# Performance work log

Hardware: AMD Instinct MI355X
Metric: run time of the kernel (lower is better)

Reference implementation:

```python
import jax, jax.numpy as jnp
import numpy as np

KH, KW = 3, 3
H_OUT, W_OUT = 62, 62

def setup_inputs() -> dict:
    key = jax.random.key(0)
    k1, k2 = jax.random.split(key)
    x = jax.random.normal(k1, (16, 32, 64, 64), dtype=jnp.float32)
    weight = jax.random.normal(k2, (H_OUT, W_OUT, 64, 32, KH, KW), dtype=jnp.float32) * 0.01
    return {"x": x, "weight": weight}

def reference(x, weight):
    # Unfold: patches[b,c,kh,kw,i,j] = x[b,c,i+kh,j+kw]; small fixed 3x3 loop is fine.
    patches = jnp.stack([
        jnp.stack([x[:, :, kh:kh + H_OUT, kw:kw + W_OUT] for kw in range(KW)], axis=2)
        for kh in range(KH)
    ], axis=2)  # [B, C_in, kH, kW, H_out, W_out]
    # Per-position (no weight sharing) contraction over c_in, kh, kw.
    out = jnp.einsum('bcklij,ijockl->boij', patches, weight)
    return jax.nn.sigmoid(out)
```

## Files before the change

kernel.cpp:

```cpp
#include <hip/hip_runtime.h>

#define HO 62
#define WO 62
#define CIN 32
#define COUT 64
#define BATCH 16
#define KROW 288
#define JT 4
#define COLS 6

typedef float f4a4 __attribute__((ext_vector_type(4), aligned(4)));

__global__ __launch_bounds__(256, 4)
void lc2d_kernel(const float* __restrict__ x,
                 const float* __restrict__ wgt,
                 float* __restrict__ out) {
    __shared__ __align__(16) float win[CIN][3][COLS][BATCH];

    const int blk = blockIdx.x;
    const int i  = blk % HO;
    const int j0 = (blk / HO) * JT;

    const int t = threadIdx.x;

    for (int r = t; r < BATCH * CIN * 3; r += 256) {
        const int b   = r & 15;
        const int ckh = r >> 4;
        const int c   = ckh / 3;
        const int kh  = ckh % 3;
        const float* src = x + (((b * CIN + c) * 64) + (i + kh)) * 64;
        #pragma unroll
        for (int cc = 0; cc < COLS; cc++) {
            int col = j0 + cc;
            if (col > 63) col = 63;
            win[c][kh][cc][b] = src[col];
        }
    }
    __syncthreads();

    const int wsel = t >> 6;
    const int o    = t & 63;

    const float* wj[JT];
    #pragma unroll
    for (int jj = 0; jj < JT; jj++) {
        int pj = i * WO + (j0 + jj);
        if (pj > HO * WO - 1) pj = HO * WO - 1;
        wj[jj] = wgt + (size_t)pj * (COUT * KROW) + o * KROW;
    }

    float acc[JT][4];
    #pragma unroll
    for (int jj = 0; jj < JT; jj++)
        #pragma unroll
        for (int bb = 0; bb < 4; bb++) acc[jj][bb] = 0.0f;

    const float* xbase = &win[0][0][0][wsel * 4];

    for (int c = 0; c < CIN; c++) {
        float wq[JT][9];
        #pragma unroll
        for (int jj = 0; jj < JT; jj++) {
            const float* p = wj[jj] + c * 9;
            const f4a4 wA = *(const f4a4*)p;
            const f4a4 wB = *(const f4a4*)(p + 4);
            wq[jj][0] = wA.x; wq[jj][1] = wA.y; wq[jj][2] = wA.z; wq[jj][3] = wA.w;
            wq[jj][4] = wB.x; wq[jj][5] = wB.y; wq[jj][6] = wB.z; wq[jj][7] = wB.w;
            wq[jj][8] = p[8];
        }
        #pragma unroll
        for (int kh = 0; kh < 3; kh++) {
            float4 xv[COLS];
            const float* xb = xbase + (c * 3 + kh) * (COLS * BATCH);
            #pragma unroll
            for (int cc = 0; cc < COLS; cc++)
                xv[cc] = *(const float4*)(xb + cc * BATCH);
            #pragma unroll
            for (int jj = 0; jj < JT; jj++) {
                #pragma unroll
                for (int kw = 0; kw < 3; kw++) {
                    const float w = wq[jj][kh * 3 + kw];
                    const float4 xx = xv[jj + kw];
                    acc[jj][0] += w * xx.x;
                    acc[jj][1] += w * xx.y;
                    acc[jj][2] += w * xx.z;
                    acc[jj][3] += w * xx.w;
                }
            }
        }
    }

    #pragma unroll
    for (int bb = 0; bb < 4; bb++) {
        const int b = wsel * 4 + bb;
        float* op = out + (((size_t)(b * COUT + o) * HO + i) * WO + j0);
        float2 s0;
        s0.x = 1.0f / (1.0f + __expf(-acc[0][bb]));
        s0.y = 1.0f / (1.0f + __expf(-acc[1][bb]));
        *(float2*)op = s0;
        if (j0 + 3 < WO) {
            float2 s1;
            s1.x = 1.0f / (1.0f + __expf(-acc[2][bb]));
            s1.y = 1.0f / (1.0f + __expf(-acc[3][bb]));
            *((float2*)op + 1) = s1;
        }
    }
}

extern "C" void kernel_launch(void* const* d_in, const int* in_sizes, int n_in,
                              void* d_out, int out_size, void* d_ws, size_t ws_size,
                              hipStream_t stream) {
    const float* x   = (const float*)d_in[0];
    const float* wgt = (const float*)d_in[1];
    float* out       = (float*)d_out;
    const int grid = HO * ((WO + JT - 1) / JT);
    lc2d_kernel<<<dim3(grid), dim3(256), 0, stream>>>(x, wgt, out);
}
```

Measured before the change: 572.0 us.

## Stage weights through double-buffered LDS with coalesced loads and two-column tiles

Weights are no longer read straight from global memory by each thread with strided per-output-channel loads. Each block now cooperatively loads 36-float chunks of the weight slab into double-buffered, padded shared memory with coalesced float4 loads, prefetching the next chunk while computing on the current one. The column tile shrinks from four to two so the grid divides evenly and no clamping is needed. This targets the weight-bandwidth-bound stream, at the cost of per-chunk syncs, more LDS use, lower occupancy and more blocks.

```diff
diff --git a/kernel.cpp b/kernel.cpp
--- a/kernel.cpp
+++ b/kernel.cpp
@@ -6,104 +6,133 @@
 #define COUT 64
 #define BATCH 16
 #define KROW 288
-#define JT 4
-#define COLS 6
+#define JT 2
+#define COLS 4
+#define NCHUNK 8
+#define CF 36
+#define WROW 37
+#define POSW (COUT * WROW)
 
-typedef float f4a4 __attribute__((ext_vector_type(4), aligned(4)));
+__device__ __forceinline__ float sigmoidf(float v) {
+    return 1.0f / (1.0f + __expf(-v));
+}
 
-__global__ __launch_bounds__(256, 4)
+__global__ __launch_bounds__(256, 2)
 void lc2d_kernel(const float* __restrict__ x,
                  const float* __restrict__ wgt,
                  float* __restrict__ out) {
     __shared__ __align__(16) float win[CIN][3][COLS][BATCH];
+    __shared__ __align__(16) float wlds[2][JT][POSW];
 
     const int blk = blockIdx.x;
     const int i  = blk % HO;
     const int j0 = (blk / HO) * JT;
-
-    const int t = threadIdx.x;
+    const int t  = threadIdx.x;
 
     for (int r = t; r < BATCH * CIN * 3; r += 256) {
         const int b   = r & 15;
         const int ckh = r >> 4;
         const int c   = ckh / 3;
-        const int kh  = ckh % 3;
-        const float* src = x + (((b * CIN + c) * 64) + (i + kh)) * 64;
+        const int kh  = ckh - c * 3;
+        const float* src = x + (((b * CIN + c) * 64) + (i + kh)) * 64 + j0;
         #pragma unroll
-        for (int cc = 0; cc < COLS; cc++) {
-            int col = j0 + cc;
-            if (col > 63) col = 63;
-            win[c][kh][cc][b] = src[col];
+        for (int cc = 0; cc < COLS; cc++)
+            win[c][kh][cc][b] = src[cc];
+    }
+
+    const int nq = (t < 128) ? 5 : 4;
+    int goff[5], loff[5];
+    #pragma unroll
+    for (int q = 0; q < 5; q++) {
+        int f = t + 256 * q;
+        if (f >= 1152) f = 1151;
+        const int pos = f / 576;
+        const int rem = f - pos * 576;
+        const int o   = rem / 9;
+        const int kk4 = rem - o * 9;
+        goff[q] = pos * (COUT * KROW) + o * KROW + kk4 * 4;
+        loff[q] = pos * POSW + o * WROW + kk4 * 4;
+    }
+    const float* wslab = wgt + (size_t)(i * WO + j0) * (COUT * KROW);
+
+    float4 st[5];
+
+    #pragma unroll
+    for (int q = 0; q < 5; q++)
+        if (q < nq) st[q] = *(const float4*)(wslab + goff[q]);
+    #pragma unroll
+    for (int q = 0; q < 5; q++)
+        if (q < nq) {
+            float* d = &wlds[0][0][0] + loff[q];
+            d[0] = st[q].x; d[1] = st[q].y; d[2] = st[q].z; d[3] = st[q].w;
         }
-    }
     __syncthreads();
 
     const int wsel = t >> 6;
     const int o    = t & 63;
+    const int bq4  = wsel * 4;
 
-    const float* wj[JT];
+    float acc0[4] = {0.f, 0.f, 0.f, 0.f};
+    float acc1[4] = {0.f, 0.f, 0.f, 0.f};
+
     #pragma unroll
-    for (int jj = 0; jj < JT; jj++) {
-        int pj = i * WO + (j0 + jj);
-        if (pj > HO * WO - 1) pj = HO * WO - 1;
-        wj[jj] = wgt + (size_t)pj * (COUT * KROW) + o * KROW;
-    }
+    for (int ch = 0; ch < NCHUNK; ch++) {
+        const int cur = ch & 1;
 
-    float acc[JT][4];
-    #pragma unroll
-    for (int jj = 0; jj < JT; jj++)
+        if (ch + 1 < NCHUNK) {
+            #pragma unroll
+            for (int q = 0; q < 5; q++)
+                if (q < nq) st[q] = *(const float4*)(wslab + goff[q] + (ch + 1) * CF);
+        }
+
+        const float* w0p = &wlds[cur][0][0] + o * WROW;
+        const float* w1p = &wlds[cur][1][0] + o * WROW;
+        float w0[CF], w1[CF];
         #pragma unroll
-        for (int bb = 0; bb < 4; bb++) acc[jj][bb] = 0.0f;
+        for (int m = 0; m < CF; m++) { w0[m] = w0p[m]; w1[m] = w1p[m]; }
 
-    const float* xbase = &win[0][0][0][wsel * 4];
-
-    for (int c = 0; c < CIN; c++) {
-        float wq[JT][9];
+        const int c0 = ch * 4;
         #pragma unroll
-        for (int jj = 0; jj < JT; jj++) {
-            const float* p = wj[jj] + c * 9;
-            const f4a4 wA = *(const f4a4*)p;
-            const f4a4 wB = *(const f4a4*)(p + 4);
-            wq[jj][0] = wA.x; wq[jj][1] = wA.y; wq[jj][2] = wA.z; wq[jj][3] = wA.w;
-            wq[jj][4] = wB.x; wq[jj][5] = wB.y; wq[jj][6] = wB.z; wq[jj][7] = wB.w;
-            wq[jj][8] = p[8];
-        }
-        #pragma unroll
-        for (int kh = 0; kh < 3; kh++) {
-            float4 xv[COLS];
-            const float* xb = xbase + (c * 3 + kh) * (COLS * BATCH);
+        for (int cl = 0; cl < 4; cl++) {
             #pragma unroll
-            for (int cc = 0; cc < COLS; cc++)
-                xv[cc] = *(const float4*)(xb + cc * BATCH);
-            #pragma unroll
-            for (int jj = 0; jj < JT; jj++) {
+            for (int kh = 0; kh < 3; kh++) {
+                const float* xb = &win[c0 + cl][kh][0][bq4];
+                float4 xv[COLS];
+                #pragma unroll
+                for (int cc = 0; cc < COLS; cc++)
+                    xv[cc] = *(const float4*)(xb + cc * BATCH);
                 #pragma unroll
                 for (int kw = 0; kw < 3; kw++) {
-                    const float w = wq[jj][kh * 3 + kw];
-                    const float4 xx = xv[jj + kw];
-                    acc[jj][0] += w * xx.x;
-                    acc[jj][1] += w * xx.y;
-                    acc[jj][2] += w * xx.z;
-                    acc[jj][3] += w * xx.w;
+                    const float wa = w0[cl * 9 + kh * 3 + kw];
+                    const float wb = w1[cl * 9 + kh * 3 + kw];
+                    acc0[0] += wa * xv[kw].x;     acc0[1] += wa * xv[kw].y;
+                    acc0[2] += wa * xv[kw].z;     acc0[3] += wa * xv[kw].w;
+                    acc1[0] += wb * xv[kw + 1].x; acc1[1] += wb * xv[kw + 1].y;
+                    acc1[2] += wb * xv[kw + 1].z; acc1[3] += wb * xv[kw + 1].w;
                 }
             }
+        }
+
+        if (ch + 1 < NCHUNK) {
+            float* base = &wlds[cur ^ 1][0][0];
+            #pragma unroll
+            for (int q = 0; q < 5; q++)
+                if (q < nq) {
+                    float* d = base + loff[q];
+                    d[0] = st[q].x; d[1] = st[q].y; d[2] = st[q].z; d[3] = st[q].w;
+                }
+            __syncthreads();
         }
     }
 
     #pragma unroll
     for (int bb = 0; bb < 4; bb++) {
-        const int b = wsel * 4 + bb;
+        const int b = bq4 + bb;
         float* op = out + (((size_t)(b * COUT + o) * HO + i) * WO + j0);
-        float2 s0;
-        s0.x = 1.0f / (1.0f + __expf(-acc[0][bb]));
-        s0.y = 1.0f / (1.0f + __expf(-acc[1][bb]));
-        *(float2*)op = s0;
-        if (j0 + 3 < WO) {
-            float2 s1;
-            s1.x = 1.0f / (1.0f + __expf(-acc[2][bb]));
-            s1.y = 1.0f / (1.0f + __expf(-acc[3][bb]));
-            *((float2*)op + 1) = s1;
-        }
+        float2 s;
+        s.x = sigmoidf(acc0[bb]);
+        s.y = sigmoidf(acc1[bb]);
+        *(float2*)op = s;
     }
 }
 
@@ -113,6 +142,6 @@
     const float* x   = (const float*)d_in[0];
     const float* wgt = (const float*)d_in[1];
     float* out       = (float*)d_out;
-    const int grid = HO * ((WO + JT - 1) / JT);
+    const int grid = HO * (WO / JT);
     lc2d_kernel<<<dim3(grid), dim3(256), 0, stream>>>(x, wgt, out);
 }
```

After: 2.226 ms. 289% more time.

## Stage weights through LDS in double-buffered chunks with coalesced global loads

Applied to the files above, without the earlier changes.

Weights were previously read straight from global memory, with each thread pulling its own 9-float row slices. Now each block loads the 288-float weight rows for its 4 output positions into shared memory in 8 chunks of 4 input channels, using contiguous 16-byte loads. The next chunk's weights and input window are prefetched into registers while the current chunk is computed. Threads are remapped so each handles one position and four output channels, and launch bounds drop to 3 waves per SIMD. The cost is more shared memory, two barriers per chunk, scalar uncoalesced output stores, and extra register pressure.

```diff
diff --git a/kernel.cpp b/kernel.cpp
--- a/kernel.cpp
+++ b/kernel.cpp
@@ -4,105 +4,155 @@
 #define WO 62
 #define CIN 32
 #define COUT 64
-#define BATCH 16
-#define KROW 288
+#define NB 16
+#define KR 288
 #define JT 4
-#define COLS 6
+#define NCH 8
+#define WROW 36
 
-typedef float f4a4 __attribute__((ext_vector_type(4), aligned(4)));
+typedef float f2 __attribute__((ext_vector_type(2)));
+typedef float f4 __attribute__((ext_vector_type(4)));
 
-__global__ __launch_bounds__(256, 4)
+__global__ __launch_bounds__(256, 3)
 void lc2d_kernel(const float* __restrict__ x,
                  const float* __restrict__ wgt,
-                 float* __restrict__ out) {
-    __shared__ __align__(16) float win[CIN][3][COLS][BATCH];
+                 float* __restrict__ out)
+{
+    __shared__ __align__(16) float wls[JT][COUT][WROW];
+    __shared__ __align__(16) float xls[4][3][6][NB];
 
     const int blk = blockIdx.x;
     const int i  = blk % HO;
     const int j0 = (blk / HO) * JT;
+    const int t  = threadIdx.x;
+    const int wv = t >> 6;
+    const int ln = t & 63;
+    const int jg = ln >> 4;
+    const int op = ln & 15;
 
-    const int t = threadIdx.x;
+    const int sp = t >> 6;
+    const int so = t & 63;
+    int pj = j0 + sp; if (pj > WO - 1) pj = WO - 1;
+    const float* wrow = wgt + ((size_t)(i * WO + pj) * COUT + so) * KR;
 
-    for (int r = t; r < BATCH * CIN * 3; r += 256) {
-        const int b   = r & 15;
-        const int ckh = r >> 4;
-        const int c   = ckh / 3;
-        const int kh  = ckh % 3;
-        const float* src = x + (((b * CIN + c) * 64) + (i + kh)) * 64;
+    const int xb  = t & 15;
+    const int xq  = t >> 4;
+    const int xcl = xq & 3;
+    const int xkh = xq >> 2;
+    int xc2 = j0 + 4; if (xc2 > 62) xc2 = 62;
+
+    f4 wst[9];
+    f4 xst4; f2 xst2;
+
+    auto loadw = [&](int ch) {
+        const float* p = wrow + ch * WROW;
         #pragma unroll
-        for (int cc = 0; cc < COLS; cc++) {
-            int col = j0 + cc;
-            if (col > 63) col = 63;
-            win[c][kh][cc][b] = src[col];
+        for (int q = 0; q < 9; q++) wst[q] = *(const f4*)(p + 4 * q);
+    };
+    auto loadx = [&](int ch) {
+        if (t < 192) {
+            const float* p = x + (((size_t)(xb * CIN + (ch * 4 + xcl)) * 64) + (i + xkh)) * 64;
+            xst4 = *(const f4*)(p + j0);
+            xst2 = *(const f2*)(p + xc2);
         }
-    }
+    };
+    auto writew = [&]() {
+        float* d = &wls[sp][so][0];
+        #pragma unroll
+        for (int q = 0; q < 9; q++) *(f4*)(d + 4 * q) = wst[q];
+    };
+    auto writex = [&]() {
+        if (t < 192) {
+            float* d = &xls[xcl][xkh][0][xb];
+            d[0 * NB] = xst4.x; d[1 * NB] = xst4.y; d[2 * NB] = xst4.z; d[3 * NB] = xst4.w;
+            d[4 * NB] = xst2.x; d[5 * NB] = xst2.y;
+        }
+    };
+
+    f4 acc[4];
+    #pragma unroll
+    for (int ko = 0; ko < 4; ko++) acc[ko] = (f4){0.f, 0.f, 0.f, 0.f};
+
+    loadw(0); loadx(0);
+    writew(); writex();
     __syncthreads();
 
-    const int wsel = t >> 6;
-    const int o    = t & 63;
+    for (int ch = 0; ch < NCH; ch++) {
+        if (ch + 1 < NCH) { loadw(ch + 1); loadx(ch + 1); }
 
-    const float* wj[JT];
-    #pragma unroll
-    for (int jj = 0; jj < JT; jj++) {
-        int pj = i * WO + (j0 + jj);
-        if (pj > HO * WO - 1) pj = HO * WO - 1;
-        wj[jj] = wgt + (size_t)pj * (COUT * KROW) + o * KROW;
-    }
+        #pragma unroll
+        for (int cl = 0; cl < 4; cl++) {
+            f4 xv[3][3];
+            #pragma unroll
+            for (int kh = 0; kh < 3; kh++)
+                #pragma unroll
+                for (int kw = 0; kw < 3; kw++)
+                    xv[kh][kw] = *(const f4*)(&xls[cl][kh][jg + kw][wv * 4]);
 
-    float acc[JT][4];
-    #pragma unroll
-    for (int jj = 0; jj < JT; jj++)
-        #pragma unroll
-        for (int bb = 0; bb < 4; bb++) acc[jj][bb] = 0.0f;
+            #pragma unroll
+            for (int ko = 0; ko < 4; ko++) {
+                const float* wr = &wls[jg][op + 16 * ko][0];
+                float wk[9];
+                if (cl == 0) {
+                    f4 a = *(const f4*)(wr);      f4 b = *(const f4*)(wr + 4);
+                    wk[0]=a.x; wk[1]=a.y; wk[2]=a.z; wk[3]=a.w;
+                    wk[4]=b.x; wk[5]=b.y; wk[6]=b.z; wk[7]=b.w;
+                    wk[8]=wr[8];
+                } else if (cl == 1) {
+                    wk[0]=wr[9];
+                    f2 a = *(const f2*)(wr + 10);
+                    f4 b = *(const f4*)(wr + 12);
+                    f2 c = *(const f2*)(wr + 16);
+                    wk[1]=a.x; wk[2]=a.y;
+                    wk[3]=b.x; wk[4]=b.y; wk[5]=b.z; wk[6]=b.w;
+                    wk[7]=c.x; wk[8]=c.y;
+                } else if (cl == 2) {
+                    f2 a = *(const f2*)(wr + 18);
+                    f4 b = *(const f4*)(wr + 20);
+                    f2 c = *(const f2*)(wr + 24);
+                    wk[0]=a.x; wk[1]=a.y;
+                    wk[2]=b.x; wk[3]=b.y; wk[4]=b.z; wk[5]=b.w;
+                    wk[6]=c.x; wk[7]=c.y;
+                    wk[8]=wr[26];
+                } else {
+                    wk[0]=wr[27];
+                    f4 a = *(const f4*)(wr + 28);  f4 b = *(const f4*)(wr + 32);
+                    wk[1]=a.x; wk[2]=a.y; wk[3]=a.z; wk[4]=a.w;
+                    wk[5]=b.x; wk[6]=b.y; wk[7]=b.z; wk[8]=b.w;
+                }
+                #pragma unroll
+                for (int kh = 0; kh < 3; kh++)
+                    #pragma unroll
+                    for (int kw = 0; kw < 3; kw++) {
+                        const float w = wk[kh * 3 + kw];
+                        acc[ko].x += w * xv[kh][kw].x;
+                        acc[ko].y += w * xv[kh][kw].y;
+                        acc[ko].z += w * xv[kh][kw].z;
+                        acc[ko].w += w * xv[kh][kw].w;
+                    }
+            }
+        }
 
-    const float* xbase = &win[0][0][0][wsel * 4];
-
-    for (int c = 0; c < CIN; c++) {
-        float wq[JT][9];
-        #pragma unroll
-        for (int jj = 0; jj < JT; jj++) {
-            const float* p = wj[jj] + c * 9;
-            const f4a4 wA = *(const f4a4*)p;
-            const f4a4 wB = *(const f4a4*)(p + 4);
-            wq[jj][0] = wA.x; wq[jj][1] = wA.y; wq[jj][2] = wA.z; wq[jj][3] = wA.w;
-            wq[jj][4] = wB.x; wq[jj][5] = wB.y; wq[jj][6] = wB.z; wq[jj][7] = wB.w;
-            wq[jj][8] = p[8];
-        }
-        #pragma unroll
-        for (int kh = 0; kh < 3; kh++) {
-            float4 xv[COLS];
-            const float* xb = xbase + (c * 3 + kh) * (COLS * BATCH);
-            #pragma unroll
-            for (int cc = 0; cc < COLS; cc++)
-                xv[cc] = *(const float4*)(xb + cc * BATCH);
-            #pragma unroll
-            for (int jj = 0; jj < JT; jj++) {
-                #pragma unroll
-                for (int kw = 0; kw < 3; kw++) {
-                    const float w = wq[jj][kh * 3 + kw];
-                    const float4 xx = xv[jj + kw];
-                    acc[jj][0] += w * xx.x;
-                    acc[jj][1] += w * xx.y;
-                    acc[jj][2] += w * xx.z;
-                    acc[jj][3] += w * xx.w;
-                }
-            }
+        if (ch + 1 < NCH) {
+            __syncthreads();
+            writew(); writex();
+            __syncthreads();
         }
     }
 
-    #pragma unroll
-    for (int bb = 0; bb < 4; bb++) {
-        const int b = wsel * 4 + bb;
-        float* op = out + (((size_t)(b * COUT + o) * HO + i) * WO + j0);
-        float2 s0;
-        s0.x = 1.0f / (1.0f + __expf(-acc[0][bb]));
-        s0.y = 1.0f / (1.0f + __expf(-acc[1][bb]));
-        *(float2*)op = s0;
-        if (j0 + 3 < WO) {
-            float2 s1;
-            s1.x = 1.0f / (1.0f + __expf(-acc[2][bb]));
-            s1.y = 1.0f / (1.0f + __expf(-acc[3][bb]));
-            *((float2*)op + 1) = s1;
+    const int j = j0 + jg;
+    if (j < WO) {
+        #pragma unroll
+        for (int ko = 0; ko < 4; ko++) {
+            const int o = op + 16 * ko;
+            #pragma unroll
+            for (int bb = 0; bb < 4; bb++) {
+                const int b = wv * 4 + bb;
+                const float v = (bb == 0) ? acc[ko].x : (bb == 1) ? acc[ko].y
+                              : (bb == 2) ? acc[ko].z : acc[ko].w;
+                out[(((size_t)(b * COUT + o) * HO) + i) * WO + j] =
+                    1.0f / (1.0f + __expf(-v));
+            }
         }
     }
 }
```

Measured after the change: 1.041 ms. 1.82x slower.

## Stream weights into LDS via async global_load_lds with double buffering

Applied to the files above, without the earlier changes.

The kernel is restructured so each block handles two output columns. The weight slab is copied into shared memory in 36-float channel chunks using the asynchronous global-to-LDS load builtin, double-buffered across chunks with a barrier per chunk. This replaces the per-thread strided 16-byte weight loads, whose accesses did not coalesce because each thread walked its own 288-float row. It adds shared-memory usage and barriers, lowers the occupancy hint to 2 and halves the columns per block, which increases the total number of blocks.

```diff
diff --git a/kernel.cpp b/kernel.cpp
--- a/kernel.cpp
+++ b/kernel.cpp
@@ -4,106 +4,148 @@
 #define WO 62
 #define CIN 32
 #define COUT 64
-#define BATCH 16
-#define KROW 288
-#define JT 4
-#define COLS 6
+#define NB 16
+#define KR 288
+#define JT 2
+#define NCH 8
+#define CHF 36
+#define POSF (COUT * KR)
+#define CHUNK_SLOTS 1152
+#define CHUNK_FLOATS 4608
 
-typedef float f4a4 __attribute__((ext_vector_type(4), aligned(4)));
+typedef float f2 __attribute__((ext_vector_type(2)));
+typedef float f4 __attribute__((ext_vector_type(4)));
 
-__global__ __launch_bounds__(256, 4)
+__device__ __forceinline__ float sigmoidf(float v) { return 1.0f / (1.0f + __expf(-v)); }
+
+__device__ __forceinline__ void dma16(const float* g, float* l) {
+    __builtin_amdgcn_global_load_lds(
+        (const __attribute__((address_space(1))) void*)g,
+        (__attribute__((address_space(3))) void*)l, 16, 0, 0);
+}
+
+__global__ __launch_bounds__(256, 2)
 void lc2d_kernel(const float* __restrict__ x,
                  const float* __restrict__ wgt,
-                 float* __restrict__ out) {
-    __shared__ __align__(16) float win[CIN][3][COLS][BATCH];
+                 float* __restrict__ out)
+{
+    __shared__ __align__(16) float wls[2][CHUNK_FLOATS];
+    __shared__ __align__(16) float xls[CIN][3][4][NB];
 
     const int blk = blockIdx.x;
     const int i  = blk % HO;
     const int j0 = (blk / HO) * JT;
+    const int t  = threadIdx.x;
+    const int wv = t >> 6;
+    const int ln = t & 63;
 
-    const int t = threadIdx.x;
+    int goff[5];
+    #pragma unroll
+    for (int s = 0; s < 5; s++) {
+        int m = t + (s << 8);
+        if (m >= CHUNK_SLOTS) m -= CHUNK_SLOTS;
+        const int pos = m / 576;
+        const int rem = m - pos * 576;
+        const int k4  = rem >> 6;
+        const int o   = rem & 63;
+        goff[s] = pos * POSF + o * KR + k4 * 4;
+    }
+    const int nS = (wv < 2) ? 5 : 4;
+    const float* wslab = wgt + (size_t)(i * WO + j0) * POSF;
 
-    for (int r = t; r < BATCH * CIN * 3; r += 256) {
+    #pragma unroll
+    for (int s = 0; s < 6; s++) {
+        const int r   = t + (s << 8);
         const int b   = r & 15;
         const int ckh = r >> 4;
         const int c   = ckh / 3;
-        const int kh  = ckh % 3;
-        const float* src = x + (((b * CIN + c) * 64) + (i + kh)) * 64;
-        #pragma unroll
-        for (int cc = 0; cc < COLS; cc++) {
-            int col = j0 + cc;
-            if (col > 63) col = 63;
-            win[c][kh][cc][b] = src[col];
-        }
+        const int kh  = ckh - c * 3;
+        const float* src = x + ((size_t)(b * CIN + c) * 64 + (i + kh)) * 64 + j0;
+        const f2 a0 = *(const f2*)(src);
+        const f2 a1 = *(const f2*)(src + 2);
+        xls[c][kh][0][b] = a0.x; xls[c][kh][1][b] = a0.y;
+        xls[c][kh][2][b] = a1.x; xls[c][kh][3][b] = a1.y;
     }
+
+    #pragma unroll
+    for (int s = 0; s < 5; s++)
+        if (s < nS)
+            dma16(wslab + goff[s], &wls[0][0] + ((((s << 2) + wv) << 6) << 2));
+
+    f4 acc0 = {0.f, 0.f, 0.f, 0.f};
+    f4 acc1 = {0.f, 0.f, 0.f, 0.f};
+
     __syncthreads();
 
-    const int wsel = t >> 6;
-    const int o    = t & 63;
+    for (int ch = 0; ch < NCH; ch++) {
+        const int cur = ch & 1;
 
-    const float* wj[JT];
-    #pragma unroll
-    for (int jj = 0; jj < JT; jj++) {
-        int pj = i * WO + (j0 + jj);
-        if (pj > HO * WO - 1) pj = HO * WO - 1;
-        wj[jj] = wgt + (size_t)pj * (COUT * KROW) + o * KROW;
-    }
+        if (ch + 1 < NCH) {
+            const float* gb = wslab + (ch + 1) * CHF;
+            #pragma unroll
+            for (int s = 0; s < 5; s++)
+                if (s < nS)
+                    dma16(gb + goff[s], &wls[cur ^ 1][0] + ((((s << 2) + wv) << 6) << 2));
+        }
 
-    float acc[JT][4];
-    #pragma unroll
-    for (int jj = 0; jj < JT; jj++)
         #pragma unroll
-        for (int bb = 0; bb < 4; bb++) acc[jj][bb] = 0.0f;
+        for (int cl = 0; cl < 4; cl++) {
+            const int c = (ch << 2) + cl;
 
-    const float* xbase = &win[0][0][0][wsel * 4];
+            f4 xv[3][4];
+            #pragma unroll
+            for (int kh = 0; kh < 3; kh++)
+                #pragma unroll
+                for (int cc = 0; cc < 4; cc++)
+                    xv[kh][cc] = *(const f4*)(&xls[c][kh][cc][wv << 2]);
 
-    for (int c = 0; c < CIN; c++) {
-        float wq[JT][9];
-        #pragma unroll
-        for (int jj = 0; jj < JT; jj++) {
-            const float* p = wj[jj] + c * 9;
-            const f4a4 wA = *(const f4a4*)p;
-            const f4a4 wB = *(const f4a4*)(p + 4);
-            wq[jj][0] = wA.x; wq[jj][1] = wA.y; wq[jj][2] = wA.z; wq[jj][3] = wA.w;
-            wq[jj][4] = wB.x; wq[jj][5] = wB.y; wq[jj][6] = wB.z; wq[jj][7] = wB.w;
-            wq[jj][8] = p[8];
-        }
-        #pragma unroll
-        for (int kh = 0; kh < 3; kh++) {
-            float4 xv[COLS];
-            const float* xb = xbase + (c * 3 + kh) * (COLS * BATCH);
+            const int g0 = (cl * 9) >> 2;
             #pragma unroll
-            for (int cc = 0; cc < COLS; cc++)
-                xv[cc] = *(const float4*)(xb + cc * BATCH);
-            #pragma unroll
-            for (int jj = 0; jj < JT; jj++) {
+            for (int jg = 0; jg < 2; jg++) {
+                const float* base = &wls[cur][jg * 2304] + (ln << 2);
+                const f4 ga = *(const f4*)(base + ((g0 + 0) << 8));
+                const f4 gb = *(const f4*)(base + ((g0 + 1) << 8));
+                const f4 gc = *(const f4*)(base + ((g0 + 2) << 8));
+                float wk[9];
+                if (cl == 0) {
+                    wk[0]=ga.x; wk[1]=ga.y; wk[2]=ga.z; wk[3]=ga.w;
+                    wk[4]=gb.x; wk[5]=gb.y; wk[6]=gb.z; wk[7]=gb.w; wk[8]=gc.x;
+                } else if (cl == 1) {
+                    wk[0]=ga.y; wk[1]=ga.z; wk[2]=ga.w;
+                    wk[3]=gb.x; wk[4]=gb.y; wk[5]=gb.z; wk[6]=gb.w;
+                    wk[7]=gc.x; wk[8]=gc.y;
+                } else if (cl == 2) {
+                    wk[0]=ga.z; wk[1]=ga.w;
+                    wk[2]=gb.x; wk[3]=gb.y; wk[4]=gb.z; wk[5]=gb.w;
+                    wk[6]=gc.x; wk[7]=gc.y; wk[8]=gc.z;
+                } else {
+                    wk[0]=ga.w;
+                    wk[1]=gb.x; wk[2]=gb.y; wk[3]=gb.z; wk[4]=gb.w;
+                    wk[5]=gc.x; wk[6]=gc.y; wk[7]=gc.z; wk[8]=gc.w;
+                }
                 #pragma unroll
-                for (int kw = 0; kw < 3; kw++) {
-                    const float w = wq[jj][kh * 3 + kw];
-                    const float4 xx = xv[jj + kw];
-                    acc[jj][0] += w * xx.x;
-                    acc[jj][1] += w * xx.y;
-                    acc[jj][2] += w * xx.z;
-                    acc[jj][3] += w * xx.w;
-                }
+                for (int kh = 0; kh < 3; kh++)
+                    #pragma unroll
+                    for (int kw = 0; kw < 3; kw++) {
+                        const float w = wk[kh * 3 + kw];
+                        if (jg == 0) acc0 += w * xv[kh][kw];
+                        else         acc1 += w * xv[kh][kw + 1];
+                    }
             }
         }
+
+        if (ch + 1 < NCH)
+            __syncthreads();
     }
 
     #pragma unroll
     for (int bb = 0; bb < 4; bb++) {
-        const int b = wsel * 4 + bb;
-        float* op = out + (((size_t)(b * COUT + o) * HO + i) * WO + j0);
-        float2 s0;
-        s0.x = 1.0f / (1.0f + __expf(-acc[0][bb]));
-        s0.y = 1.0f / (1.0f + __expf(-acc[1][bb]));
-        *(float2*)op = s0;
-        if (j0 + 3 < WO) {
-            float2 s1;
-            s1.x = 1.0f / (1.0f + __expf(-acc[2][bb]));
-            s1.y = 1.0f / (1.0f + __expf(-acc[3][bb]));
-            *((float2*)op + 1) = s1;
-        }
+        const int b = (wv << 2) + bb;
+        float* op = out + ((size_t)(b * COUT + ln) * HO + i) * WO + j0;
+        const float v0 = (bb == 0) ? acc0.x : (bb == 1) ? acc0.y : (bb == 2) ? acc0.z : acc0.w;
+        const float v1 = (bb == 0) ? acc1.x : (bb == 1) ? acc1.y : (bb == 2) ? acc1.z : acc1.w;
+        f2 s; s.x = sigmoidf(v0); s.y = sigmoidf(v1);
+        *(f2*)op = s;
     }
 }
 
@@ -113,6 +155,6 @@
     const float* x   = (const float*)d_in[0];
     const float* wgt = (const float*)d_in[1];
     float* out       = (float*)d_out;
-    const int grid = HO * ((WO + JT - 1) / JT);
+    const int grid = HO * (WO / JT);
     lc2d_kernel<<<dim3(grid), dim3(256), 0, stream>>>(x, wgt, out);
 }
```

After: 1.884 ms. +229.4%, slower.
